# Optimization experiments

Hardware: AMD Instinct MI355X
Metric: run time of the kernel (lower is better)

The kernel has to match this reference:

```python
import jax, jax.numpy as jnp
import numpy as np

B, P = 4, 50000
D_IN, COND = 3, 48
# layer l: in IN_DIMS[l] -> out OUT_DIMS[l]; dims=[3,256*8,257], skip at layer index 4
IN_DIMS  = [D_IN + COND, 256, 256, 256, 256, 256, 256, 256, 256]
OUT_DIMS = [256, 256, 256, 253, 256, 256, 256, 256, 257]
N_LIN = 9
INV_SQRT2 = np.float32(1.0 / np.sqrt(2.0))


def softplus_beta100(x):
    return jax.nn.softplus(100.0 * x) * 0.01


def setup_inputs() -> dict:
    key = jax.random.key(0)
    ks = jax.random.split(key, 2 + 2 * N_LIN)
    inp = {
        "input": jax.random.normal(ks[0], (B, P, D_IN), dtype=jnp.float32),
        "cond_pose": jax.random.normal(ks[1], (B, COND), dtype=jnp.float32),
    }
    for l in range(N_LIN):
        scale = np.float32(np.sqrt(2.0 / OUT_DIMS[l]))  # geometry-style init scale
        inp[f"W{l}"] = jax.random.normal(ks[2 + 2 * l], (OUT_DIMS[l], IN_DIMS[l]), dtype=jnp.float32) * scale
        inp[f"b{l}"] = jnp.zeros((OUT_DIMS[l],), dtype=jnp.float32)
    return inp


def reference(input, cond_pose,
              W0, b0, W1, b1, W2, b2, W3, b3, W4, b4, W5, b5, W6, b6, W7, b7, W8, b8):
    Ws = [W0, W1, W2, W3, W4, W5, W6, W7, W8]
    bs = [b0, b1, b2, b3, b4, b5, b6, b7, b8]
    nb, npnt, nd = input.shape
    x_in = input.reshape(nb * npnt, nd)                                   # (N, 3)
    c = jnp.broadcast_to(cond_pose[:, None, :], (nb, npnt, COND)).reshape(nb * npnt, COND)
    x = jnp.concatenate([x_in, c], axis=-1)                               # cond concat at layer 0
    for l in range(N_LIN):
        if l == 4:  # skip connection: concat raw input, scaled by 1/sqrt(2)
            x = jnp.concatenate([x, x_in], axis=-1) * INV_SQRT2
        x = x @ Ws[l].T + bs[l]
        if l < N_LIN - 1:
            x = softplus_beta100(x)
    return x.reshape(nb, npnt, -1)                                        # (B, P, 257)
```

## Files before the change

### kernel.cpp

```cpp
#include <hip/hip_runtime.h>


typedef __attribute__((ext_vector_type(8))) short bf16x8;
typedef __attribute__((ext_vector_type(4))) short s16x4;
typedef __attribute__((ext_vector_type(4))) float f32x4;

#define PPTS 50000

__device__ __forceinline__ short f2bf(float f) {
    union { float f; unsigned u; } v; v.f = f;
    unsigned r = v.u + 0x7fffu + ((v.u >> 16) & 1u);
    return (short)(r >> 16);
}

__device__ __forceinline__ float softplus100(float x) {
    float e = __builtin_amdgcn_exp2f(fabsf(x) * -144.26950408889634f);
    float l = __builtin_amdgcn_logf(1.0f + e);
    return fmaxf(x, 0.0f) + 0.0069314718055994531f * l;
}

__device__ __forceinline__ short* xaddr(short* base, int row, int col) {
    int off = ((row << 9) + (col << 1)) ^ ((row & 7) << 4);
    return (short*)((char*)base + off);
}
__device__ __forceinline__ const short* xaddrc(const short* base, int row, int col) {
    int off = ((row << 9) + (col << 1)) ^ ((row & 7) << 4);
    return (const short*)((const char*)base + off);
}

__global__ void prep_kernel(
    const float* __restrict__ W0, const float* __restrict__ W1, const float* __restrict__ W2,
    const float* __restrict__ W3, const float* __restrict__ W4, const float* __restrict__ W5,
    const float* __restrict__ W6, const float* __restrict__ W7, const float* __restrict__ W8,
    short* __restrict__ wbf)
{
    const int gid = blockIdx.x * blockDim.x + threadIdx.x;
    if (gid >= 68096) return;
    int l, cid; const float* Wsrc;
    if      (gid <  2048) { l = 0; cid = gid;         Wsrc = W0; }
    else if (gid < 10240) { l = 1; cid = gid -  2048; Wsrc = W1; }
    else if (gid < 18432) { l = 2; cid = gid - 10240; Wsrc = W2; }
    else if (gid < 26624) { l = 3; cid = gid - 18432; Wsrc = W3; }
    else if (gid < 34816) { l = 4; cid = gid - 26624; Wsrc = W4; }
    else if (gid < 43008) { l = 5; cid = gid - 34816; Wsrc = W5; }
    else if (gid < 51200) { l = 6; cid = gid - 43008; Wsrc = W6; }
    else if (gid < 59392) { l = 7; cid = gid - 51200; Wsrc = W7; }
    else                  { l = 8; cid = gid - 59392; Wsrc = W8; }
    const int NR   = (l == 3) ? 253 : ((l == 8) ? 257 : 256);
    const int KR   = (l == 0) ? 51 : 256;
    const int klog = (l == 0) ? 1 : 3;
    const int lane  = cid & 63;
    const int tile  = cid >> 6;
    const int ntile = tile >> klog;
    const int ktile = tile & ((1 << klog) - 1);
    const int n  = ntile * 16 + (lane & 15);
    const int k0 = ktile * 32 + ((lane >> 4) << 3);
    bf16x8 v;
#pragma unroll
    for (int j = 0; j < 8; ++j) {
        int k = k0 + j;
        float f = (n < NR && k < KR) ? Wsrc[n * KR + k] : 0.0f;
        v[j] = f2bf(f);
    }
    ((bf16x8*)wbf)[gid] = v;
}

template<int KSTEPS, int MODE>
__device__ __forceinline__ void layer_fwd(const short* src, short* dst,
    const bf16x8* __restrict__ wl, const float* __restrict__ bias, int lane, int wid)
{
    const int prow = lane & 15;
    const int kg   = (lane >> 4) << 3;
    const int rb4  = (lane >> 4) << 2;
    f32x4 bv[2];
#pragma unroll
    for (int nii = 0; nii < 2; ++nii) {
        const int cb = (wid * 2 + nii) * 16 + rb4;
        if (MODE == 1 && cb == 252) { f32x4 t = {bias[252], 0.f, 0.f, 0.f}; bv[nii] = t; }
        else bv[nii] = *(const f32x4*)(bias + cb);
    }
    f32x4 acc[4][2] = {};
#pragma unroll 2
    for (int ks = 0; ks < KSTEPS; ++ks) {
        bf16x8 a[2], b[4];
#pragma unroll
        for (int nii = 0; nii < 2; ++nii)
            a[nii] = wl[((wid * 2 + nii) * KSTEPS + ks) * 64 + lane];
#pragma unroll
        for (int mi = 0; mi < 4; ++mi)
            b[mi] = *(const bf16x8*)xaddrc(src, mi * 16 + prow, ks * 32 + kg);
#pragma unroll
        for (int mi = 0; mi < 4; ++mi)
#pragma unroll
            for (int nii = 0; nii < 2; ++nii)
                acc[mi][nii] = __builtin_amdgcn_mfma_f32_16x16x32_bf16(
                    a[nii], b[mi], acc[mi][nii], 0, 0, 0);
    }
#pragma unroll
    for (int nii = 0; nii < 2; ++nii) {
        const int cb = (wid * 2 + nii) * 16 + rb4;
#pragma unroll
        for (int mi = 0; mi < 4; ++mi) {
            s16x4 p;
#pragma unroll
            for (int r = 0; r < 4; ++r) {
                float s = softplus100(acc[mi][nii][r] + bv[nii][r]);
                if (MODE == 1) s *= 0.70710678f;
                p[r] = f2bf(s);
            }
            if (MODE == 1 && cb == 252)
                *xaddr(dst, mi * 16 + prow, 252) = p[0];
            else
                *(s16x4*)xaddr(dst, mi * 16 + prow, cb) = p;
        }
    }
}

__global__ __launch_bounds__(512, 4) void net_kernel(
    const float* __restrict__ xin, const float* __restrict__ cond,
    const bf16x8* __restrict__ W,
    const float* __restrict__ b0, const float* __restrict__ b1, const float* __restrict__ b2,
    const float* __restrict__ b3, const float* __restrict__ b4, const float* __restrict__ b5,
    const float* __restrict__ b6, const float* __restrict__ b7, const float* __restrict__ b8,
    float* __restrict__ out)
{
    __shared__ short xb0[64 * 256];
    __shared__ short xb1[64 * 256];
    const int t    = threadIdx.x;
    const int pt0  = blockIdx.x * 64;
    const int lane = t & 63;
    const int wid  = t >> 6;

    float sk[3] = {0.f, 0.f, 0.f};
    if (t < 64) {
#pragma unroll
        for (int c = 0; c < 3; ++c)
            sk[c] = xin[(pt0 + t) * 3 + c] * 0.70710678f;
    }

    {
        const int row   = t >> 3;
        const int c0    = (t & 7) << 3;
        const int point = pt0 + row;
        const int batch = point / PPTS;
        const float* xp = xin + point * 3;
        const float* cp = cond + batch * 48;
        bf16x8 v;
#pragma unroll
        for (int i = 0; i < 8; ++i) {
            int c = c0 + i;
            float f = (c < 3) ? xp[c] : ((c < 51) ? cp[c - 3] : 0.0f);
            v[i] = f2bf(f);
        }
        *(bf16x8*)xaddr(xb0, row, c0) = v;
    }
    __syncthreads();

    layer_fwd<2, 0>(xb0, xb1, W +     0, b0, lane, wid); __syncthreads();
    layer_fwd<8, 0>(xb1, xb0, W +  2048, b1, lane, wid); __syncthreads();
    layer_fwd<8, 0>(xb0, xb1, W + 10240, b2, lane, wid); __syncthreads();
    layer_fwd<8, 1>(xb1, xb0, W + 18432, b3, lane, wid);
    if (t < 64) {
#pragma unroll
        for (int c = 0; c < 3; ++c)
            *xaddr(xb0, t, 253 + c) = f2bf(sk[c]);
    }
    __syncthreads();
    layer_fwd<8, 0>(xb0, xb1, W + 26624, b4, lane, wid); __syncthreads();
    layer_fwd<8, 0>(xb1, xb0, W + 34816, b5, lane, wid); __syncthreads();
    layer_fwd<8, 0>(xb0, xb1, W + 43008, b6, lane, wid); __syncthreads();
    layer_fwd<8, 0>(xb1, xb0, W + 51200, b7, lane, wid); __syncthreads();

    {
        const bf16x8* wl = W + 59392;
        const int prow = lane & 15;
        const int kg   = (lane >> 4) << 3;
        const int rb4  = (lane >> 4) << 2;
        f32x4 acc[4][2] = {};
        f32x4 acc2[4]   = {};
#pragma unroll 2
        for (int ks = 0; ks < 8; ++ks) {
            bf16x8 a[2], b[4];
#pragma unroll
            for (int nii = 0; nii < 2; ++nii)
                a[nii] = wl[((wid * 2 + nii) * 8 + ks) * 64 + lane];
            bf16x8 a2;
            if (wid == 0) a2 = wl[(128 + ks) * 64 + lane];
#pragma unroll
            for (int mi = 0; mi < 4; ++mi)
                b[mi] = *(const bf16x8*)xaddrc(xb0, mi * 16 + prow, ks * 32 + kg);
#pragma unroll
            for (int mi = 0; mi < 4; ++mi) {
#pragma unroll
                for (int nii = 0; nii < 2; ++nii)
                    acc[mi][nii] = __builtin_amdgcn_mfma_f32_16x16x32_bf16(
                        a[nii], b[mi], acc[mi][nii], 0, 0, 0);
            }
            if (wid == 0) {
#pragma unroll
                for (int mi = 0; mi < 4; ++mi)
                    acc2[mi] = __builtin_amdgcn_mfma_f32_16x16x32_bf16(
                        a2, b[mi], acc2[mi], 0, 0, 0);
            }
        }
#pragma unroll
        for (int nii = 0; nii < 2; ++nii) {
            const int cb = (wid * 2 + nii) * 16 + rb4;
            const f32x4 bv = *(const f32x4*)(b8 + cb);
#pragma unroll
            for (int mi = 0; mi < 4; ++mi) {
                const int rowoff = (pt0 + mi * 16 + prow) * 257 + cb;
#pragma unroll
                for (int r = 0; r < 4; ++r)
                    out[rowoff + r] = acc[mi][nii][r] + bv[r];
            }
        }
        if (wid == 0 && rb4 == 0) {
            const float blast = b8[256];
#pragma unroll
            for (int mi = 0; mi < 4; ++mi)
                out[(pt0 + mi * 16 + prow) * 257 + 256] = acc2[mi][0] + blast;
        }
    }
}

extern "C" void kernel_launch(void* const* d_in, const int* in_sizes, int n_in,
                              void* d_out, int out_size, void* d_ws, size_t ws_size,
                              hipStream_t stream)
{
    const float* xin  = (const float*)d_in[0];
    const float* cond = (const float*)d_in[1];
    const float* Wp[9]; const float* bp[9];
    for (int l = 0; l < 9; ++l) { Wp[l] = (const float*)d_in[2 + 2 * l]; bp[l] = (const float*)d_in[3 + 2 * l]; }
    short* wbf = (short*)d_ws;

    prep_kernel<<<dim3(266), dim3(256), 0, stream>>>(
        Wp[0], Wp[1], Wp[2], Wp[3], Wp[4], Wp[5], Wp[6], Wp[7], Wp[8], wbf);
    net_kernel<<<dim3(3125), dim3(512), 0, stream>>>(
        xin, cond, (const bf16x8*)wbf,
        bp[0], bp[1], bp[2], bp[3], bp[4], bp[5], bp[6], bp[7], bp[8],
        (float*)d_out);
}
```

Before: 316.1 us.

## Use single in-place LDS activation buffer, polynomial softplus, packed bf16 convert

Activations now live in one shared buffer updated in place, with a barrier between the matrix-multiply reads and the epilogue writes. This halves LDS use, and launch bounds are raised to allow more resident blocks per CU. The softplus log is replaced by a cubic polynomial in exp(-|x|), and bf16 packing uses the hardware v_cvt_pk_bf16_f32 instruction. The risks are register pressure or spills from the tighter launch bound, an extra barrier per layer, and small numerical differences from the approximation.

```diff
diff --git a/kernel.cpp b/kernel.cpp
--- a/kernel.cpp
+++ b/kernel.cpp
@@ -2,7 +2,6 @@
 
 
 typedef __attribute__((ext_vector_type(8))) short bf16x8;
-typedef __attribute__((ext_vector_type(4))) short s16x4;
 typedef __attribute__((ext_vector_type(4))) float f32x4;
 
 #define PPTS 50000
@@ -13,10 +12,18 @@
     return (short)(r >> 16);
 }
 
+__device__ __forceinline__ unsigned cvt_pk_bf16(float lo, float hi) {
+    unsigned r;
+    asm("v_cvt_pk_bf16_f32 %0, %1, %2" : "=v"(r) : "v"(lo), "v"(hi));
+    return r;
+}
+
 __device__ __forceinline__ float softplus100(float x) {
+    const float A = 6.9314718e-3f, B = -3.11522e-3f, C = 9.8829e-4f;
     float e = __builtin_amdgcn_exp2f(fabsf(x) * -144.26950408889634f);
-    float l = __builtin_amdgcn_logf(1.0f + e);
-    return fmaxf(x, 0.0f) + 0.0069314718055994531f * l;
+    float t = __builtin_fmaf(C, e, B);
+    t = __builtin_fmaf(t, e, A);
+    return __builtin_fmaf(e, t, fmaxf(x, 0.0f));
 }
 
 __device__ __forceinline__ short* xaddr(short* base, int row, int col) {
@@ -66,7 +73,7 @@
 }
 
 template<int KSTEPS, int MODE>
-__device__ __forceinline__ void layer_fwd(const short* src, short* dst,
+__device__ __forceinline__ void layer_fwd(short* xb,
     const bf16x8* __restrict__ wl, const float* __restrict__ bias, int lane, int wid)
 {
     const int prow = lane & 15;
@@ -88,7 +95,7 @@
             a[nii] = wl[((wid * 2 + nii) * KSTEPS + ks) * 64 + lane];
 #pragma unroll
         for (int mi = 0; mi < 4; ++mi)
-            b[mi] = *(const bf16x8*)xaddrc(src, mi * 16 + prow, ks * 32 + kg);
+            b[mi] = *(const bf16x8*)xaddrc(xb, mi * 16 + prow, ks * 32 + kg);
 #pragma unroll
         for (int mi = 0; mi < 4; ++mi)
 #pragma unroll
@@ -96,27 +103,32 @@
                 acc[mi][nii] = __builtin_amdgcn_mfma_f32_16x16x32_bf16(
                     a[nii], b[mi], acc[mi][nii], 0, 0, 0);
     }
+    __syncthreads();
 #pragma unroll
     for (int nii = 0; nii < 2; ++nii) {
         const int cb = (wid * 2 + nii) * 16 + rb4;
 #pragma unroll
         for (int mi = 0; mi < 4; ++mi) {
-            s16x4 p;
+            float s[4];
 #pragma unroll
             for (int r = 0; r < 4; ++r) {
-                float s = softplus100(acc[mi][nii][r] + bv[nii][r]);
-                if (MODE == 1) s *= 0.70710678f;
-                p[r] = f2bf(s);
-            }
-            if (MODE == 1 && cb == 252)
-                *xaddr(dst, mi * 16 + prow, 252) = p[0];
-            else
-                *(s16x4*)xaddr(dst, mi * 16 + prow, cb) = p;
-        }
-    }
-}
-
-__global__ __launch_bounds__(512, 4) void net_kernel(
+                float v = softplus100(acc[mi][nii][r] + bv[nii][r]);
+                if (MODE == 1) v *= 0.70710678f;
+                s[r] = v;
+            }
+            unsigned p01 = cvt_pk_bf16(s[0], s[1]);
+            unsigned p23 = cvt_pk_bf16(s[2], s[3]);
+            if (MODE == 1 && cb == 252) {
+                *xaddr(xb, mi * 16 + prow, 252) = (short)(p01 & 0xffff);
+            } else {
+                uint2 pk; pk.x = p01; pk.y = p23;
+                *(uint2*)xaddr(xb, mi * 16 + prow, cb) = pk;
+            }
+        }
+    }
+}
+
+__global__ __launch_bounds__(512, 8) void net_kernel(
     const float* __restrict__ xin, const float* __restrict__ cond,
     const bf16x8* __restrict__ W,
     const float* __restrict__ b0, const float* __restrict__ b1, const float* __restrict__ b2,
@@ -124,8 +136,7 @@
     const float* __restrict__ b6, const float* __restrict__ b7, const float* __restrict__ b8,
     float* __restrict__ out)
 {
-    __shared__ short xb0[64 * 256];
-    __shared__ short xb1[64 * 256];
+    __shared__ short xb[64 * 256];
     const int t    = threadIdx.x;
     const int pt0  = blockIdx.x * 64;
     const int lane = t & 63;
@@ -152,24 +163,24 @@
             float f = (c < 3) ? xp[c] : ((c < 51) ? cp[c - 3] : 0.0f);
             v[i] = f2bf(f);
         }
-        *(bf16x8*)xaddr(xb0, row, c0) = v;
+        *(bf16x8*)xaddr(xb, row, c0) = v;
     }
     __syncthreads();
 
-    layer_fwd<2, 0>(xb0, xb1, W +     0, b0, lane, wid); __syncthreads();
-    layer_fwd<8, 0>(xb1, xb0, W +  2048, b1, lane, wid); __syncthreads();
-    layer_fwd<8, 0>(xb0, xb1, W + 10240, b2, lane, wid); __syncthreads();
-    layer_fwd<8, 1>(xb1, xb0, W + 18432, b3, lane, wid);
+    layer_fwd<2, 0>(xb, W +     0, b0, lane, wid); __syncthreads();
+    layer_fwd<8, 0>(xb, W +  2048, b1, lane, wid); __syncthreads();
+    layer_fwd<8, 0>(xb, W + 10240, b2, lane, wid); __syncthreads();
+    layer_fwd<8, 1>(xb, W + 18432, b3, lane, wid);
     if (t < 64) {
 #pragma unroll
         for (int c = 0; c < 3; ++c)
-            *xaddr(xb0, t, 253 + c) = f2bf(sk[c]);
+            *xaddr(xb, t, 253 + c) = f2bf(sk[c]);
     }
     __syncthreads();
-    layer_fwd<8, 0>(xb0, xb1, W + 26624, b4, lane, wid); __syncthreads();
-    layer_fwd<8, 0>(xb1, xb0, W + 34816, b5, lane, wid); __syncthreads();
-    layer_fwd<8, 0>(xb0, xb1, W + 43008, b6, lane, wid); __syncthreads();
-    layer_fwd<8, 0>(xb1, xb0, W + 51200, b7, lane, wid); __syncthreads();
+    layer_fwd<8, 0>(xb, W + 26624, b4, lane, wid); __syncthreads();
+    layer_fwd<8, 0>(xb, W + 34816, b5, lane, wid); __syncthreads();
+    layer_fwd<8, 0>(xb, W + 43008, b6, lane, wid); __syncthreads();
+    layer_fwd<8, 0>(xb, W + 51200, b7, lane, wid); __syncthreads();
 
     {
         const bf16x8* wl = W + 59392;
@@ -188,7 +199,7 @@
             if (wid == 0) a2 = wl[(128 + ks) * 64 + lane];
 #pragma unroll
             for (int mi = 0; mi < 4; ++mi)
-                b[mi] = *(const bf16x8*)xaddrc(xb0, mi * 16 + prow, ks * 32 + kg);
+                b[mi] = *(const bf16x8*)xaddrc(xb, mi * 16 + prow, ks * 32 + kg);
 #pragma unroll
             for (int mi = 0; mi < 4; ++mi) {
 #pragma unroll
```

New measurement: 491.4 us. +55.5%, slower.
